# Kernel optimization log

Measured on AMD Instinct MI355X. Metric: run time of the kernel, lower is better.

The kernel has to match this reference:

```python
import jax, jax.numpy as jnp
import numpy as np

NUM_EXPERTS = 8
TOP_K = 2
HIDDEN = 1024
NUM_TOKENS = 8192


def setup_inputs() -> dict:
    key = jax.random.key(0)
    k1, k2, k3 = jax.random.split(key, 3)
    x = jax.random.normal(k1, (NUM_TOKENS, HIDDEN), dtype=jnp.float32)
    # gate: nn.Linear(hidden, num_experts, bias=False) -> weight [E, H]
    gate_w = jax.random.normal(k2, (NUM_EXPERTS, HIDDEN), dtype=jnp.float32) * 0.02
    # experts: nn.Linear(hidden, hidden, bias=False) stacked -> [E, H_out, H_in]
    expert_w = jax.random.normal(k3, (NUM_EXPERTS, HIDDEN, HIDDEN), dtype=jnp.float32) * 0.02
    return {"x": x, "gate_w": gate_w, "expert_w": expert_w}


def reference(x, gate_w, expert_w):
    # --- routing ---
    logits = jnp.einsum("th,eh->te", x, gate_w)          # [T, E]
    probs = jax.nn.softmax(logits, axis=-1)
    weights, indices = jax.lax.top_k(probs, TOP_K)        # [T, K], [T, K]

    # --- expert compute (equivalent of dispatch + per-expert GEMM) ---
    # y_e = x @ W_e^T for every expert; tokens then gather their top-k rows.
    all_y = jnp.einsum("td,ehd->eth", x, expert_w)        # [E, T, H]

    # --- weighted combine (gather by routed expert ids) ---
    t_idx = jnp.arange(x.shape[0])[None, :]               # [1, T]
    y_sel = all_y[indices.T, t_idx, :]                    # [K, T, H]
    out = jnp.einsum("tk,kth->th", weights, y_sel)        # [T, H]
    return out
```

## Files before the change

### kernel.cpp

```cpp
#include <hip/hip_runtime.h>
#include <hip/hip_bf16.h>
#include <stdint.h>

#define NUM_TOKENS 8192
#define HIDDEN 1024
#define NEXP 8
#define TOPK 2

typedef __bf16 bf16;
typedef __bf16 bf16x4 __attribute__((ext_vector_type(4)));
typedef __bf16 bf16x8 __attribute__((ext_vector_type(8)));
typedef float f32x4 __attribute__((ext_vector_type(4)));

__device__ __forceinline__ void gld_lds16(const void* g, void* l) {
  __builtin_amdgcn_global_load_lds(
      (const __attribute__((address_space(1))) void*)(uintptr_t)g,
      (__attribute__((address_space(3))) void*)(uint32_t)(uintptr_t)l,
      16, 0, 0);
}

__global__ __launch_bounds__(256) void prep_kernel(
    const float* __restrict__ x, const float* __restrict__ gw,
    const float* __restrict__ ew,
    bf16* __restrict__ xbf, bf16* __restrict__ wbf,
    int* __restrict__ echoice, float* __restrict__ pchoice,
    float* __restrict__ out)
{
  const int b   = blockIdx.x;
  const int tid = threadIdx.x;

  if (b < 2048) {
    const int wid  = tid >> 6;
    const int lane = tid & 63;
    const int t = b * 4 + wid;

    const float* xrow = x + (size_t)t * HIDDEN;
    bf16* xbrow = xbf + (size_t)t * HIDDEN;

    float acc[NEXP];
#pragma unroll
    for (int e = 0; e < NEXP; ++e) acc[e] = 0.f;

#pragma unroll
    for (int it = 0; it < 4; ++it) {
      const int idx = it * 256 + lane * 4;
      float4 xv = *(const float4*)(xrow + idx);
      bf16x4 xb;
      xb[0] = (bf16)xv.x; xb[1] = (bf16)xv.y; xb[2] = (bf16)xv.z; xb[3] = (bf16)xv.w;
      *(bf16x4*)(xbrow + idx) = xb;
#pragma unroll
      for (int e = 0; e < NEXP; ++e) {
        float4 gv = *(const float4*)(gw + e * HIDDEN + idx);
        acc[e] += xv.x * gv.x + xv.y * gv.y + xv.z * gv.z + xv.w * gv.w;
      }
    }
#pragma unroll
    for (int e = 0; e < NEXP; ++e) {
#pragma unroll
      for (int off = 32; off > 0; off >>= 1)
        acc[e] += __shfl_xor(acc[e], off, 64);
    }

    if (lane == 0) {
      float m = acc[0];
#pragma unroll
      for (int e = 1; e < NEXP; ++e) m = fmaxf(m, acc[e]);
      float p[NEXP]; float s = 0.f;
#pragma unroll
      for (int e = 0; e < NEXP; ++e) { p[e] = expf(acc[e] - m); s += p[e]; }
      const float inv = 1.f / s;
#pragma unroll
      for (int e = 0; e < NEXP; ++e) p[e] *= inv;
      int i0 = 0; float p0 = p[0];
#pragma unroll
      for (int e = 1; e < NEXP; ++e) if (p[e] > p0) { p0 = p[e]; i0 = e; }
      int i1 = -1; float p1 = -1.f;
#pragma unroll
      for (int e = 0; e < NEXP; ++e) if (e != i0 && p[e] > p1) { p1 = p[e]; i1 = e; }

      echoice[t]              = i0;
      echoice[NUM_TOKENS + t] = i1;
      pchoice[t]              = p0;
      pchoice[NUM_TOKENS + t] = p1;
    }
  } else if (b < 4096) {
    const size_t i = ((size_t)(b - 2048) * 256 + tid) * 16;
    float4 v0 = *(const float4*)(ew + i);
    float4 v1 = *(const float4*)(ew + i + 4);
    float4 v2 = *(const float4*)(ew + i + 8);
    float4 v3 = *(const float4*)(ew + i + 12);
    bf16x8 o0, o1;
    o0[0] = (bf16)v0.x; o0[1] = (bf16)v0.y; o0[2] = (bf16)v0.z; o0[3] = (bf16)v0.w;
    o0[4] = (bf16)v1.x; o0[5] = (bf16)v1.y; o0[6] = (bf16)v1.z; o0[7] = (bf16)v1.w;
    o1[0] = (bf16)v2.x; o1[1] = (bf16)v2.y; o1[2] = (bf16)v2.z; o1[3] = (bf16)v2.w;
    o1[4] = (bf16)v3.x; o1[5] = (bf16)v3.y; o1[6] = (bf16)v3.z; o1[7] = (bf16)v3.w;
    *(bf16x8*)(wbf + i)     = o0;
    *(bf16x8*)(wbf + i + 8) = o1;
  } else {
    const size_t i = ((size_t)(b - 4096) * 256 + tid) * 16;
    const float4 z = {0.f, 0.f, 0.f, 0.f};
    *(float4*)(out + i)      = z;
    *(float4*)(out + i + 4)  = z;
    *(float4*)(out + i + 8)  = z;
    *(float4*)(out + i + 12) = z;
  }
}

__global__ __launch_bounds__(1024) void build_lists_kernel(
    const int* __restrict__ echoice, const float* __restrict__ pchoice,
    int* __restrict__ cnt, int* __restrict__ tok, float* __restrict__ wt)
{
  const int list = blockIdx.x;
  const int k = list >> 3;
  const int e = list & 7;
  const int tid  = threadIdx.x;
  const int wave = tid >> 6;
  const int lane = tid & 63;
  const int tbase = wave * 512;

  const int*   ec = echoice + k * NUM_TOKENS;
  const float* pc = pchoice + k * NUM_TOKENS;

  __shared__ int wcnt[16];
  __shared__ int woff[16];

  const unsigned long long lower = ((unsigned long long)1 << lane) - 1;

  int   ev[8];
  float pv[8];
#pragma unroll
  for (int c = 0; c < 8; ++c) {
    ev[c] = ec[tbase + c * 64 + lane];
    pv[c] = pc[tbase + c * 64 + lane];
  }
  unsigned long long m[8];
  int cl = 0;
#pragma unroll
  for (int c = 0; c < 8; ++c) { m[c] = __ballot(ev[c] == e); cl += __popcll(m[c]); }
  if (lane == 0) wcnt[wave] = cl;
  __syncthreads();
  if (tid == 0) {
    int off = 0;
#pragma unroll
    for (int w = 0; w < 16; ++w) { woff[w] = off; off += wcnt[w]; }
    cnt[list] = off;
  }
  __syncthreads();
  int run = woff[wave];
#pragma unroll
  for (int c = 0; c < 8; ++c) {
    if (ev[c] == e) {
      const int pos = run + __popcll(m[c] & lower);
      tok[(size_t)list * NUM_TOKENS + pos] = tbase + c * 64 + lane;
      wt [(size_t)list * NUM_TOKENS + pos] = pv[c];
    }
    run += __popcll(m[c]);
  }
}

__global__ __launch_bounds__(256, 4) void moe_gemm_kernel(
    const bf16* __restrict__ xbf, const bf16* __restrict__ wbf,
    const int* __restrict__ cnt, const int* __restrict__ tok,
    const float* __restrict__ wt, float* __restrict__ out)
{
  const int e  = blockIdx.x & 7;
  const int g  = blockIdx.x >> 3;
  const int nt = g & 7;
  const int mt = (g >> 3) & 63;
  const int k  = g >> 9;
  const int list = k * NEXP + e;
  const int count = cnt[list];
  const int m0 = mt * 128;
  if (m0 >= count) return;
  const int rows = min(128, count - m0);

  __shared__ __align__(16) bf16 As[2][128 * 32];
  __shared__ __align__(16) bf16 Bs[2][128 * 32];
  __shared__ int   tok_s[128];
  __shared__ float wt_s[128];

  const int tid = threadIdx.x;
  if (tid < 128) {
    if (tid < rows) {
      tok_s[tid] = tok[(size_t)list * NUM_TOKENS + m0 + tid];
      wt_s[tid]  = wt [(size_t)list * NUM_TOKENS + m0 + tid];
    } else { tok_s[tid] = 0; wt_s[tid] = 0.f; }
  }
  __syncthreads();

  const int csrc = (((tid & 3) ^ ((tid >> 3) & 3)) << 3);
  const int r0 = tid >> 2;
  const bf16* gA0 = xbf + (size_t)tok_s[r0] * HIDDEN + csrc;
  const bf16* gA1 = xbf + (size_t)tok_s[r0 + 64] * HIDDEN + csrc;
  const bf16* gB0 = wbf + (size_t)e * HIDDEN * HIDDEN
                  + (size_t)(nt * 128 + r0) * HIDDEN + csrc;
  const bf16* gB1 = gB0 + (size_t)64 * HIDDEN;

  auto STAGE = [&](int t, int buf) {
    const int kc = t << 5;
    bf16* la = &As[buf][0] + tid * 8;
    bf16* lb = &Bs[buf][0] + tid * 8;
    gld_lds16(gA0 + kc, la);
    gld_lds16(gA1 + kc, la + 2048);
    gld_lds16(gB0 + kc, lb);
    gld_lds16(gB1 + kc, lb + 2048);
  };

  const int wid  = tid >> 6;
  const int lane = tid & 63;
  const int wm = (wid >> 1) * 64;
  const int wn = (wid & 1) * 64;
  const int qm = lane & 15;
  const int l4 = lane >> 4;

  f32x4 acc[4][4];
#pragma unroll
  for (int i = 0; i < 4; ++i)
#pragma unroll
    for (int j = 0; j < 4; ++j) acc[i][j] = (f32x4){0.f, 0.f, 0.f, 0.f};

  auto COMPUTE = [&](int buf) {
    const bf16* Ab = &As[buf][0];
    const bf16* Bb = &Bs[buf][0];
    bf16x8 a[4], b[4];
#pragma unroll
    for (int i = 0; i < 4; ++i) {
      const int r = wm + i * 16 + qm;
      a[i] = *(const bf16x8*)(Ab + r * 32 + ((l4 ^ ((r >> 1) & 3)) << 3));
    }
#pragma unroll
    for (int j = 0; j < 4; ++j) {
      const int r = wn + j * 16 + qm;
      b[j] = *(const bf16x8*)(Bb + r * 32 + ((l4 ^ ((r >> 1) & 3)) << 3));
    }
    __builtin_amdgcn_s_setprio(1);
#pragma unroll
    for (int i = 0; i < 4; ++i)
#pragma unroll
      for (int j = 0; j < 4; ++j)
        acc[i][j] = __builtin_amdgcn_mfma_f32_16x16x32_bf16(a[i], b[j], acc[i][j], 0, 0, 0);
    __builtin_amdgcn_s_setprio(0);
  };

  STAGE(0, 0);
  __syncthreads();
#pragma unroll 1
  for (int t = 0; t < 32; ++t) {
    if (t < 31) STAGE(t + 1, (t + 1) & 1);
    COMPUTE(t & 1);
    if (t < 31) __syncthreads();
  }

  const int h0 = nt * 128 + wn + qm;
#pragma unroll
  for (int i = 0; i < 4; ++i) {
    const int rbase = wm + i * 16 + (lane >> 4) * 4;
#pragma unroll
    for (int r = 0; r < 4; ++r) {
      const int rl = rbase + r;
      if (rl < rows) {
        const int t = tok_s[rl];
        const float w = wt_s[rl];
        float* orow = out + (size_t)t * HIDDEN + h0;
#pragma unroll
        for (int j = 0; j < 4; ++j) {
          const float v = w * acc[i][j][r];
          unsafeAtomicAdd(orow + j * 16, v);
        }
      }
    }
  }
}

extern "C" void kernel_launch(void* const* d_in, const int* in_sizes, int n_in,
                              void* d_out, int out_size, void* d_ws, size_t ws_size,
                              hipStream_t stream) {
  const float* x  = (const float*)d_in[0];
  const float* gw = (const float*)d_in[1];
  const float* ew = (const float*)d_in[2];
  float* out = (float*)d_out;

  char* ws = (char*)d_ws;
  int*   cnt     = (int*)ws;
  int*   echoice = (int*)(ws + 256);
  float* pchoice = (float*)(ws + 256 + (size_t)2 * NUM_TOKENS * 4);
  int*   tok = (int*)(ws + 256 + (size_t)4 * NUM_TOKENS * 4);
  float* wt  = (float*)(ws + 256 + (size_t)20 * NUM_TOKENS * 4);
  bf16*  xbf = (bf16*)(ws + 256 + (size_t)36 * NUM_TOKENS * 4);
  bf16*  wbf = (bf16*)((char*)xbf + (size_t)NUM_TOKENS * HIDDEN * 2);

  prep_kernel<<<6144, 256, 0, stream>>>(x, gw, ew, xbf, wbf, echoice, pchoice, out);
  build_lists_kernel<<<2 * NEXP, 1024, 0, stream>>>(echoice, pchoice, cnt, tok, wt);

  moe_gemm_kernel<<<8192, 256, 0, stream>>>(xbf, wbf, cnt, tok, wt, out);
}
```

Baseline: 206.2 us.

## Replace sparse 8192-block grid with compact work queue and persistent GEMM blocks

Adds a single-block kernel that builds a dense list of the (expert, slot, m-tile, n-tile) work items that are actually populated, interleaved by expert. The GEMM becomes a persistent kernel of 1024 blocks that stride through this queue. Previously most of the 8192 launched blocks exited early. The aim is to remove that launch and early-exit overhead and to spread tiles evenly across CUs. In exchange it adds an extra kernel launch, serializes the queue build on one block, and uses a fixed stride that can leave tail imbalance.

```diff
diff --git a/kernel.cpp b/kernel.cpp
--- a/kernel.cpp
+++ b/kernel.cpp
@@ -158,53 +158,45 @@
   }
 }
 
+__global__ __launch_bounds__(256) void build_work_kernel(
+    const int* __restrict__ cnt, int* __restrict__ work, int* __restrict__ nw)
+{
+  __shared__ int t0s[8], t1s[8];
+  const int tid = threadIdx.x;
+  if (tid < 8) {
+    t0s[tid] = (cnt[tid] + 127) >> 7;
+    t1s[tid] = (cnt[tid + 8] + 127) >> 7;
+  }
+  __syncthreads();
+  int mx = 0;
+#pragma unroll
+  for (int e = 0; e < NEXP; ++e) mx = max(mx, (t0s[e] + t1s[e]) * 8);
+  if (tid == 0) nw[0] = mx * 8;
+  for (int p = tid; p < mx * 8; p += 256) {
+    const int e = p & 7;
+    const int j = p >> 3;
+    const int tile = j >> 3;
+    const int nt = j & 7;
+    int w = -1;
+    if (tile < t0s[e])              w = (e << 9) | (tile << 3) | nt;
+    else if (tile < t0s[e] + t1s[e]) w = ((e + 8) << 9) | ((tile - t0s[e]) << 3) | nt;
+    work[p] = w;
+  }
+}
+
 __global__ __launch_bounds__(256, 4) void moe_gemm_kernel(
     const bf16* __restrict__ xbf, const bf16* __restrict__ wbf,
     const int* __restrict__ cnt, const int* __restrict__ tok,
-    const float* __restrict__ wt, float* __restrict__ out)
+    const float* __restrict__ wt, const int* __restrict__ work,
+    const int* __restrict__ nw, float* __restrict__ out)
 {
-  const int e  = blockIdx.x & 7;
-  const int g  = blockIdx.x >> 3;
-  const int nt = g & 7;
-  const int mt = (g >> 3) & 63;
-  const int k  = g >> 9;
-  const int list = k * NEXP + e;
-  const int count = cnt[list];
-  const int m0 = mt * 128;
-  if (m0 >= count) return;
-  const int rows = min(128, count - m0);
-
   __shared__ __align__(16) bf16 As[2][128 * 32];
   __shared__ __align__(16) bf16 Bs[2][128 * 32];
   __shared__ int   tok_s[128];
   __shared__ float wt_s[128];
 
   const int tid = threadIdx.x;
-  if (tid < 128) {
-    if (tid < rows) {
-      tok_s[tid] = tok[(size_t)list * NUM_TOKENS + m0 + tid];
-      wt_s[tid]  = wt [(size_t)list * NUM_TOKENS + m0 + tid];
-    } else { tok_s[tid] = 0; wt_s[tid] = 0.f; }
-  }
-  __syncthreads();
-
-  const int csrc = (((tid & 3) ^ ((tid >> 3) & 3)) << 3);
-  const int r0 = tid >> 2;
-  const bf16* gA0 = xbf + (size_t)tok_s[r0] * HIDDEN + csrc;
-  const bf16* gA1 = xbf + (size_t)tok_s[r0 + 64] * HIDDEN + csrc;
-  const bf16* gB0 = wbf + (size_t)e * HIDDEN * HIDDEN
-                  + (size_t)(nt * 128 + r0) * HIDDEN + csrc;
-  const bf16* gB1 = gB0 + (size_t)64 * HIDDEN;
-
-  auto STAGE = [&](int t, int buf) {
-    const int kc = t << 5;
-    bf16* la = &As[buf][0] + tid * 8;
-    bf16* lb = &Bs[buf][0] + tid * 8;
-    gld_lds16(gA0 + kc, la);
-    gld_lds16(gA1 + kc, la + 2048);
-    gld_lds16(gB0 + kc, lb);
-    gld_lds16(gB1 + kc, lb + 2048);
-  };
+  const int nwork = nw[0];
 
   const int wid  = tid >> 6;
   const int lane = tid & 63;
@@ -212,60 +204,100 @@
   const int wn = (wid & 1) * 64;
   const int qm = lane & 15;
   const int l4 = lane >> 4;
-
-  f32x4 acc[4][4];
-#pragma unroll
-  for (int i = 0; i < 4; ++i)
-#pragma unroll
-    for (int j = 0; j < 4; ++j) acc[i][j] = (f32x4){0.f, 0.f, 0.f, 0.f};
-
-  auto COMPUTE = [&](int buf) {
-    const bf16* Ab = &As[buf][0];
-    const bf16* Bb = &Bs[buf][0];
-    bf16x8 a[4], b[4];
+  const int csrc = (((tid & 3) ^ ((tid >> 3) & 3)) << 3);
+  const int r0 = tid >> 2;
+
+#pragma unroll 1
+  for (int idx = blockIdx.x; idx < nwork; idx += 1024) {
+    const int w = work[idx];
+    if (w < 0) continue;
+    const int nt   = w & 7;
+    const int mt   = (w >> 3) & 63;
+    const int list = (w >> 9) & 15;
+    const int e    = list & 7;
+    const int count = cnt[list];
+    const int m0 = mt * 128;
+    const int rows = min(128, count - m0);
+
+    __syncthreads();
+    if (tid < 128) {
+      if (tid < rows) {
+        tok_s[tid] = tok[(size_t)list * NUM_TOKENS + m0 + tid];
+        wt_s[tid]  = wt [(size_t)list * NUM_TOKENS + m0 + tid];
+      } else { tok_s[tid] = 0; wt_s[tid] = 0.f; }
+    }
+    __syncthreads();
+
+    const bf16* gA0 = xbf + (size_t)tok_s[r0] * HIDDEN + csrc;
+    const bf16* gA1 = xbf + (size_t)tok_s[r0 + 64] * HIDDEN + csrc;
+    const bf16* gB0 = wbf + (size_t)e * HIDDEN * HIDDEN
+                    + (size_t)(nt * 128 + r0) * HIDDEN + csrc;
+    const bf16* gB1 = gB0 + (size_t)64 * HIDDEN;
+
+    auto STAGE = [&](int t, int buf) {
+      const int kc = t << 5;
+      bf16* la = &As[buf][0] + tid * 8;
+      bf16* lb = &Bs[buf][0] + tid * 8;
+      gld_lds16(gA0 + kc, la);
+      gld_lds16(gA1 + kc, la + 2048);
+      gld_lds16(gB0 + kc, lb);
+      gld_lds16(gB1 + kc, lb + 2048);
+    };
+
+    f32x4 acc[4][4];
+#pragma unroll
+    for (int i = 0; i < 4; ++i)
+#pragma unroll
+      for (int j = 0; j < 4; ++j) acc[i][j] = (f32x4){0.f, 0.f, 0.f, 0.f};
+
+    auto COMPUTE = [&](int buf) {
+      const bf16* Ab = &As[buf][0];
+      const bf16* Bb = &Bs[buf][0];
+      bf16x8 a[4], b[4];
+#pragma unroll
+      for (int i = 0; i < 4; ++i) {
+        const int r = wm + i * 16 + qm;
+        a[i] = *(const bf16x8*)(Ab + r * 32 + ((l4 ^ ((r >> 1) & 3)) << 3));
+      }
+#pragma unroll
+      for (int j = 0; j < 4; ++j) {
+        const int r = wn + j * 16 + qm;
+        b[j] = *(const bf16x8*)(Bb + r * 32 + ((l4 ^ ((r >> 1) & 3)) << 3));
+      }
+      __builtin_amdgcn_s_setprio(1);
+#pragma unroll
+      for (int i = 0; i < 4; ++i)
+#pragma unroll
+        for (int j = 0; j < 4; ++j)
+          acc[i][j] = __builtin_amdgcn_mfma_f32_16x16x32_bf16(a[i], b[j], acc[i][j], 0, 0, 0);
+      __builtin_amdgcn_s_setprio(0);
+    };
+
+    STAGE(0, 0);
+    __syncthreads();
+#pragma unroll 1
+    for (int t = 0; t < 32; ++t) {
+      if (t < 31) STAGE(t + 1, (t + 1) & 1);
+      COMPUTE(t & 1);
+      if (t < 31) __syncthreads();
+    }
+
+    const int h0 = nt * 128 + wn + qm;
 #pragma unroll
     for (int i = 0; i < 4; ++i) {
-      const int r = wm + i * 16 + qm;
-      a[i] = *(const bf16x8*)(Ab + r * 32 + ((l4 ^ ((r >> 1) & 3)) << 3));
-    }
-#pragma unroll
-    for (int j = 0; j < 4; ++j) {
-      const int r = wn + j * 16 + qm;
-      b[j] = *(const bf16x8*)(Bb + r * 32 + ((l4 ^ ((r >> 1) & 3)) << 3));
-    }
-    __builtin_amdgcn_s_setprio(1);
-#pragma unroll
-    for (int i = 0; i < 4; ++i)
-#pragma unroll
-      for (int j = 0; j < 4; ++j)
-        acc[i][j] = __builtin_amdgcn_mfma_f32_16x16x32_bf16(a[i], b[j], acc[i][j], 0, 0, 0);
-    __builtin_amdgcn_s_setprio(0);
-  };
-
-  STAGE(0, 0);
-  __syncthreads();
-#pragma unroll 1
-  for (int t = 0; t < 32; ++t) {
-    if (t < 31) STAGE(t + 1, (t + 1) & 1);
-    COMPUTE(t & 1);
-    if (t < 31) __syncthreads();
-  }
-
-  const int h0 = nt * 128 + wn + qm;
-#pragma unroll
-  for (int i = 0; i < 4; ++i) {
-    const int rbase = wm + i * 16 + (lane >> 4) * 4;
-#pragma unroll
-    for (int r = 0; r < 4; ++r) {
-      const int rl = rbase + r;
-      if (rl < rows) {
-        const int t = tok_s[rl];
-        const float w = wt_s[rl];
-        float* orow = out + (size_t)t * HIDDEN + h0;
-#pragma unroll
-        for (int j = 0; j < 4; ++j) {
-          const float v = w * acc[i][j][r];
-          unsafeAtomicAdd(orow + j * 16, v);
+      const int rbase = wm + i * 16 + (lane >> 4) * 4;
+#pragma unroll
+      for (int r = 0; r < 4; ++r) {
+        const int rl = rbase + r;
+        if (rl < rows) {
+          const int t = tok_s[rl];
+          const float wgt = wt_s[rl];
+          float* orow = out + (size_t)t * HIDDEN + h0;
+#pragma unroll
+          for (int j = 0; j < 4; ++j) {
+            const float v = wgt * acc[i][j][r];
+            unsafeAtomicAdd(orow + j * 16, v);
+          }
         }
       }
     }
@@ -282,15 +314,18 @@
 
   char* ws = (char*)d_ws;
   int*   cnt     = (int*)ws;
+  int*   nwg     = cnt + 16;
   int*   echoice = (int*)(ws + 256);
   float* pchoice = (float*)(ws + 256 + (size_t)2 * NUM_TOKENS * 4);
   int*   tok = (int*)(ws + 256 + (size_t)4 * NUM_TOKENS * 4);
   float* wt  = (float*)(ws + 256 + (size_t)20 * NUM_TOKENS * 4);
-  bf16*  xbf = (bf16*)(ws + 256 + (size_t)36 * NUM_TOKENS * 4);
+  int*   workq = (int*)(ws + 256 + (size_t)36 * NUM_TOKENS * 4);
+  bf16*  xbf = (bf16*)(ws + 256 + (size_t)36 * NUM_TOKENS * 4 + 32768);
   bf16*  wbf = (bf16*)((char*)xbf + (size_t)NUM_TOKENS * HIDDEN * 2);
 
   prep_kernel<<<6144, 256, 0, stream>>>(x, gw, ew, xbf, wbf, echoice, pchoice, out);
   build_lists_kernel<<<2 * NEXP, 1024, 0, stream>>>(echoice, pchoice, cnt, tok, wt);
-
-  moe_gemm_kernel<<<8192, 256, 0, stream>>>(xbf, wbf, cnt, tok, wt, out);
-}
+  build_work_kernel<<<1, 256, 0, stream>>>(cnt, workq, nwg);
+
+  moe_gemm_kernel<<<1024, 256, 0, stream>>>(xbf, wbf, cnt, tok, wt, workq, nwg, out);
+}
```

After: 208.0 us. About the same (+0.9%).
